# Kernel optimization log

Measured on AMD Instinct MI355X. Metric: run time of the kernel, lower is better.

The kernel has to match this reference:

```python
import jax, jax.numpy as jnp
import numpy as np

N_OBJ, N_EVT, N_EDGE, N_MAIN = 50000, 100000, 500000, 25000
OBJ_DIM, EVT_DIM = 256, 256


def setup_inputs() -> dict:
    key = jax.random.key(0)
    ks = jax.random.split(key, 12)
    s = 1.0 / np.sqrt(OBJ_DIM)
    return {
        "object_X": jax.random.normal(ks[0], (N_OBJ, OBJ_DIM), jnp.float32),
        "event_X": jax.random.normal(ks[1], (N_EVT, EVT_DIM), jnp.float32),
        "lc_obj_idx": jax.random.randint(ks[2], (N_EDGE,), 0, N_OBJ),
        "lc_evt_idx": jax.random.randint(ks[3], (N_EDGE,), 0, N_EVT),
        "main_idx": jax.random.randint(ks[4], (N_MAIN,), 0, N_OBJ),
        # lifecycle_proj: Linear(event_dim, obj_dim)
        "W_proj": jax.random.uniform(ks[5], (OBJ_DIM, EVT_DIM), jnp.float32, -s, s),
        "b_proj": jax.random.uniform(ks[6], (OBJ_DIM,), jnp.float32, -s, s),
        # GRUCell(obj_dim, obj_dim): weight_ih/hh are [3*H, H]
        "W_ih": jax.random.uniform(ks[7], (3 * OBJ_DIM, OBJ_DIM), jnp.float32, -s, s),
        "b_ih": jax.random.uniform(ks[8], (3 * OBJ_DIM,), jnp.float32, -s, s),
        "W_hh": jax.random.uniform(ks[9], (3 * OBJ_DIM, OBJ_DIM), jnp.float32, -s, s),
        "b_hh": jax.random.uniform(ks[10], (3 * OBJ_DIM,), jnp.float32, -s, s),
    }


def reference(object_X, event_X, lc_obj_idx, lc_evt_idx, main_idx,
              W_proj, b_proj, W_ih, b_ih, W_hh, b_hh):
    n_obj = object_X.shape[0]
    # gather event feats, linear + ReLU  -> [E, obj_dim]
    proj = jax.nn.relu(event_X[lc_evt_idx] @ W_proj.T + b_proj)
    # scatter_mean over target objects (empty slots -> 0, like torch_scatter)
    sums = jax.ops.segment_sum(proj, lc_obj_idx, num_segments=n_obj)
    cnt = jax.ops.segment_sum(jnp.ones((lc_obj_idx.shape[0],), proj.dtype),
                              lc_obj_idx, num_segments=n_obj)
    profile = sums / jnp.maximum(cnt, 1.0)[:, None]  # [N_obj, obj_dim]
    # GRUCell(profile, object_X)
    gi = profile @ W_ih.T + b_ih   # [N_obj, 3H]
    gh = object_X @ W_hh.T + b_hh  # [N_obj, 3H]
    i_r, i_z, i_n = jnp.split(gi, 3, axis=-1)
    h_r, h_z, h_n = jnp.split(gh, 3, axis=-1)
    r = jax.nn.sigmoid(i_r + h_r)
    z = jax.nn.sigmoid(i_z + h_z)
    n = jnp.tanh(i_n + r * h_n)
    updated = (1.0 - z) * n + z * object_X
    # masked blend: only main objects take updated values
    mask = jnp.zeros((n_obj, 1), object_X.dtype).at[main_idx].set(1.0)
    return mask * updated + (1.0 - mask) * object_X
```

## Files before the change

kernel.cpp:

```cpp
#include <hip/hip_runtime.h>

typedef unsigned short u16;
typedef __attribute__((ext_vector_type(8))) short bf16x8;
typedef __attribute__((ext_vector_type(4))) float f32x4;

struct __align__(8) u16x4_t { u16 x, y, z, w; };

__device__ __forceinline__ float b2f(u16 b) {
  union { unsigned u; float f; } v; v.u = ((unsigned)b) << 16; return v.f;
}
__device__ __forceinline__ u16 f2b(float f) {
  union { float f; unsigned u; } v; v.f = f;
  unsigned r = v.u + 0x7fffu + ((v.u >> 16) & 1u);
  return (u16)(r >> 16);
}
__device__ __forceinline__ unsigned pk2(float lo, float hi) {
  unsigned r;
  asm("v_cvt_pk_bf16_f32 %0, %1, %2" : "=v"(r) : "v"(lo), "v"(hi));
  return r;
}

__global__ void prep(const float* __restrict__ Wp, const float* __restrict__ Wi,
                     const float* __restrict__ Wh, u16* __restrict__ wb,
                     const int* __restrict__ main_idx, int* __restrict__ mask,
                     int* __restrict__ mlist, int* __restrict__ cpos,
                     int* __restrict__ mcount, int nMain) {
  int b = blockIdx.x;
  if (b < 448) {
    int t = b * 256 + threadIdx.x;
    const float* src; int o;
    if (t < 16384)      { src = Wp; o = t; }
    else if (t < 65536) { src = Wi; o = t - 16384; }
    else                { src = Wh; o = t - 65536; }
    float4 v = ((const float4*)src)[o];
    u16x4_t q;
    q.x = f2b(v.x); q.y = f2b(v.y); q.z = f2b(v.z); q.w = f2b(v.w);
    ((u16x4_t*)wb)[t] = q;
  } else {
    int t = (b - 448) * 256 + threadIdx.x;
    if (t < nMain) {
      int o = main_idx[t];
      if (atomicCAS(&mask[o], 0, 1) == 0) {
        int i = atomicAdd(mcount, 1);
        mlist[i] = o;
        cpos[o] = i;
      }
    }
  }
}

__global__ void count_edges(const int* __restrict__ obj_idx, const int* __restrict__ mask,
                            int* __restrict__ deg, int n) {
  int e = blockIdx.x * 256 + threadIdx.x;
  if (e >= n) return;
  int o = obj_idx[e];
  if (mask[o]) atomicAdd(&deg[o], 1);
}

__global__ __launch_bounds__(256)
void alloc_offs(const int* __restrict__ mlist, const int* __restrict__ mcount,
                const int* __restrict__ deg, int* __restrict__ offs,
                int* __restrict__ tcur, int* __restrict__ rrows, int Mpad) {
  int i = blockIdx.x * 256 + threadIdx.x;
  int lane = threadIdx.x & 63;
  int mc = *mcount;
  if (i < Mpad) rrows[i] = (i < mc) ? mlist[i] : 0;
  int o = (i < mc) ? mlist[i] : 0;
  int d = (i < mc) ? deg[o] : 0;
  int x = d;
#pragma unroll
  for (int s = 1; s < 64; s <<= 1) {
    int y = __shfl_up(x, s, 64);
    if (lane >= s) x += y;
  }
  int wt = __shfl(x, 63, 64);
  int base = 0;
  if (lane == 63 && wt > 0) base = atomicAdd(tcur, wt);
  base = __shfl(base, 63, 64);
  if (i < mc) offs[o] = base + (x - d);
}

__global__ void fill_edges(const int* __restrict__ obj_idx, const int* __restrict__ evt_idx,
                           const int* __restrict__ mask, const int* __restrict__ offs,
                           int* __restrict__ cursor, int* __restrict__ elist, int n) {
  int e = blockIdx.x * 256 + threadIdx.x;
  if (e >= n) return;
  int o = obj_idx[e];
  if (!mask[o]) return;
  int pos = atomicAdd(&cursor[o], 1);
  elist[offs[o] + pos] = evt_idx[e];
}

__global__ __launch_bounds__(256)
void accum_gather(const u16* __restrict__ P, const int* __restrict__ elist,
                  const int* __restrict__ offs, const int* __restrict__ deg,
                  const int* __restrict__ mlist, const int* __restrict__ mcount,
                  const float* __restrict__ objX, const int* __restrict__ rrows,
                  u16* __restrict__ prof, u16* __restrict__ objc, int Mpad) {
  const int wave = threadIdx.x >> 6;
  const int lane = threadIdx.x & 63;
  const int i = blockIdx.x * 4 + wave;
  if (i >= Mpad) return;

  int src = rrows[i];
  float4 xv = *(const float4*)(objX + (size_t)src * 256 + lane * 4);

  const int mc = *mcount;
  float a0 = 0.f, a1 = 0.f, a2 = 0.f, a3 = 0.f;
  int d = 0;
  if (i < mc) {
    const int o = mlist[i];
    const int off = offs[o];
    d = deg[o];
    int j = 0;
    for (; j + 1 < d; j += 2) {
      int e0 = elist[off + j], e1 = elist[off + j + 1];
      u16x4_t p0 = *(const u16x4_t*)(P + (size_t)e0 * 256 + lane * 4);
      u16x4_t p1 = *(const u16x4_t*)(P + (size_t)e1 * 256 + lane * 4);
      a0 += b2f(p0.x) + b2f(p1.x);
      a1 += b2f(p0.y) + b2f(p1.y);
      a2 += b2f(p0.z) + b2f(p1.z);
      a3 += b2f(p0.w) + b2f(p1.w);
    }
    if (j < d) {
      int e0 = elist[off + j];
      u16x4_t p0 = *(const u16x4_t*)(P + (size_t)e0 * 256 + lane * 4);
      a0 += b2f(p0.x); a1 += b2f(p0.y); a2 += b2f(p0.z); a3 += b2f(p0.w);
    }
  }
  float s = 1.f / fmaxf((float)d, 1.f);
  u16x4_t pv;
  pv.x = f2b(a0 * s); pv.y = f2b(a1 * s); pv.z = f2b(a2 * s); pv.w = f2b(a3 * s);
  *(u16x4_t*)(prof + (size_t)i * 256 + lane * 4) = pv;

  u16x4_t ov;
  ov.x = f2b(xv.x); ov.y = f2b(xv.y); ov.z = f2b(xv.z); ov.w = f2b(xv.w);
  *(u16x4_t*)(objc + (size_t)i * 256 + lane * 4) = ov;
}

template<int RELU>
__device__ __forceinline__
void gemm_core(const u16* __restrict__ A, const u16* __restrict__ B,
               const float* __restrict__ bias, u16* __restrict__ C,
               int M, int N, int n0, int m0, u16* lA, u16* lB) {
  const int tid  = threadIdx.x;
  const int lane = tid & 63;
  const int wave = tid >> 6;
  const int mR = (wave & 1) * 64;
  const int nC = (wave >> 1) * 64;

  int srow[4], skq[4];
#pragma unroll
  for (int s = 0; s < 4; ++s) {
    int g = s * 256 + tid;
    srow[s] = g >> 3;
    skq[s]  = ((g & 7) ^ ((g >> 3) & 7)) << 3;
  }

  f32x4 acc[4][4] = {};

  auto STAGE = [&](int buf, int kt) {
#pragma unroll
    for (int s = 0; s < 4; ++s) {
      int row = srow[s];
      int ar = m0 + row; ar = (ar < M) ? ar : (M - 1);
      const u16* gA = A + (size_t)ar * 256 + kt + skq[s];
      __builtin_amdgcn_global_load_lds(
          (const __attribute__((address_space(1))) void*)gA,
          (__attribute__((address_space(3))) void*)(lA + buf * 8192 + s * 2048 + wave * 512),
          16, 0, 0);
      const u16* gB = B + (size_t)(n0 + row) * 256 + kt + skq[s];
      __builtin_amdgcn_global_load_lds(
          (const __attribute__((address_space(1))) void*)gB,
          (__attribute__((address_space(3))) void*)(lB + buf * 8192 + s * 2048 + wave * 512),
          16, 0, 0);
    }
  };

  STAGE(0, 0);
  __syncthreads();

  for (int t = 0; t < 4; ++t) {
    const int cur = t & 1;
    if (t < 3) STAGE(cur ^ 1, (t + 1) * 64);
    const u16* bA = lA + cur * 8192;
    const u16* bB = lB + cur * 8192;
#pragma unroll
    for (int ks = 0; ks < 2; ++ks) {
      const int kbq = ks * 4 + (lane >> 4);
      bf16x8 af[4], bf[4];
#pragma unroll
      for (int i = 0; i < 4; ++i) {
        int ra = mR + i * 16 + (lane & 15);
        af[i] = *(const bf16x8*)(bA + ra * 64 + ((kbq ^ (ra & 7)) << 3));
        int rb = nC + i * 16 + (lane & 15);
        bf[i] = *(const bf16x8*)(bB + rb * 64 + ((kbq ^ (rb & 7)) << 3));
      }
#pragma unroll
      for (int i = 0; i < 4; ++i)
#pragma unroll
        for (int j = 0; j < 4; ++j)
          acc[i][j] = __builtin_amdgcn_mfma_f32_16x16x32_bf16(af[i], bf[j], acc[i][j], 0, 0, 0);
    }
    __syncthreads();
  }

  const int crow = (lane >> 4) * 4;
  const int ccol = lane & 15;
#pragma unroll
  for (int i = 0; i < 4; ++i) {
#pragma unroll
    for (int j = 0; j < 4; ++j) {
      int col = n0 + nC + j * 16 + ccol;
      float bv = bias[col];
#pragma unroll
      for (int q = 0; q < 4; ++q) {
        int row = m0 + mR + i * 16 + crow + q;
        if (row < M) {
          float v = acc[i][j][q] + bv;
          if (RELU) v = fmaxf(v, 0.f);
          C[(size_t)row * N + col] = f2b(v);
        }
      }
    }
  }
}

__device__ __forceinline__ int xcd_swz(int bid, int nwg) {
  int q = nwg >> 3, r = nwg & 7;
  int xcd = bid & 7, loc = bid >> 3;
  return (xcd < r ? xcd * (q + 1) : r * (q + 1) + (xcd - r) * q) + loc;
}

__global__ __launch_bounds__(256, 2)
void gemm_pf(const float* __restrict__ A, const u16* __restrict__ B,
             const float* __restrict__ bias, u16* __restrict__ C, int M) {
  __shared__ float lA[2][64 * 32];
  __shared__ u16   lB[2][128 * 64];
  const int tid  = threadIdx.x;
  const int lane = tid & 63;
  const int wave = tid >> 6;
  const int m0 = blockIdx.x * 64;
  const int nC = wave * 64;

  const float* asrc[2];
  const u16*   bsrc[4];
#pragma unroll
  for (int s = 0; s < 2; ++s) {
    int g = s * 256 + tid;
    int row = g >> 3, qp = g & 7;
    int q = qp ^ (row & 7);
    int ar = m0 + row; ar = (ar < M) ? ar : (M - 1);
    asrc[s] = A + (size_t)ar * 256 + q * 4;
  }
#pragma unroll
  for (int s = 0; s < 4; ++s) {
    int g = s * 256 + tid;
    int rp = g >> 3, qp = g & 7;
    int bq = qp ^ (rp & 7);
    int n  = rp * 2 + (bq >> 2);
    bsrc[s] = B + (size_t)n * 256 + (bq & 3) * 8;
  }

  auto STAGE = [&](int buf, int kt) {
#pragma unroll
    for (int s = 0; s < 2; ++s) {
      int g = s * 256 + tid;
      __builtin_amdgcn_global_load_lds(
          (const __attribute__((address_space(1))) void*)(asrc[s] + kt),
          (__attribute__((address_space(3))) void*)(&lA[buf][g * 4]),
          16, 0, 0);
    }
#pragma unroll
    for (int s = 0; s < 4; ++s) {
      int g = s * 256 + tid;
      __builtin_amdgcn_global_load_lds(
          (const __attribute__((address_space(1))) void*)(bsrc[s] + kt),
          (__attribute__((address_space(3))) void*)(&lB[buf][g * 8]),
          16, 0, 0);
    }
  };

  f32x4 acc[4][4] = {};
  STAGE(0, 0);
  __syncthreads();

  const int h = lane >> 4;
  for (int t = 0; t < 8; ++t) {
    const int cur = t & 1;
    if (t < 7) STAGE(cur ^ 1, (t + 1) * 32);
    const float* bA = lA[cur];
    const u16*   bB = lB[cur];
    bf16x8 af[4], bf[4];
#pragma unroll
    for (int i = 0; i < 4; ++i) {
      int ra = i * 16 + (lane & 15);
      int pg = (2 * h) ^ (ra & 7);
      float4 x = *(const float4*)(bA + ra * 32 + pg * 4);
      float4 y = *(const float4*)(bA + ra * 32 + (pg ^ 1) * 4);
      union { unsigned u[4]; bf16x8 v; } cv;
      cv.u[0] = pk2(x.x, x.y); cv.u[1] = pk2(x.z, x.w);
      cv.u[2] = pk2(y.x, y.y); cv.u[3] = pk2(y.z, y.w);
      af[i] = cv.v;
    }
#pragma unroll
    for (int j = 0; j < 4; ++j) {
      int rb = nC + j * 16 + (lane & 15);
      int qp = (((rb & 1) << 2) | h) ^ ((rb >> 1) & 7);
      bf[j] = *(const bf16x8*)(bB + (rb >> 1) * 64 + qp * 8);
    }
#pragma unroll
    for (int i = 0; i < 4; ++i)
#pragma unroll
      for (int j = 0; j < 4; ++j)
        acc[i][j] = __builtin_amdgcn_mfma_f32_16x16x32_bf16(af[i], bf[j], acc[i][j], 0, 0, 0);
    __syncthreads();
  }

  const int crow = (lane >> 4) * 4;
  const int ccol = lane & 15;
#pragma unroll
  for (int i = 0; i < 4; ++i) {
#pragma unroll
    for (int j = 0; j < 4; ++j) {
      int col = nC + j * 16 + ccol;
      float bv = bias[col];
#pragma unroll
      for (int q = 0; q < 4; ++q) {
        int row = m0 + i * 16 + crow + q;
        if (row < M)
          C[(size_t)row * 256 + col] = f2b(fmaxf(acc[i][j][q] + bv, 0.f));
      }
    }
  }
}

__global__ __launch_bounds__(256, 2)
void gemm2_dual(const u16* __restrict__ prof, const u16* __restrict__ objc,
                const u16* __restrict__ wib, const u16* __restrict__ whb,
                const float* __restrict__ bi, const float* __restrict__ bh,
                u16* __restrict__ gi, u16* __restrict__ gh, int Mpad, int nwg) {
  __shared__ u16 lA[2 * 8192];
  __shared__ u16 lB[2 * 8192];
  int wg = xcd_swz(blockIdx.x, nwg);
  int m0 = (wg / 12) * 128;
  int y = wg % 12;
  if (y < 6) gemm_core<0>(prof, wib, bi, gi, Mpad, 768, y * 128, m0, lA, lB);
  else       gemm_core<0>(objc, whb, bh, gh, Mpad, 768, (y - 6) * 128, m0, lA, lB);
}

__global__ __launch_bounds__(256)
void gate_out(const u16* __restrict__ gi, const u16* __restrict__ gh,
              const float* __restrict__ objX, const int* __restrict__ mask,
              const int* __restrict__ cpos, float* __restrict__ out, int nObj) {
  const int wave = threadIdx.x >> 6;
  const int lane = threadIdx.x & 63;
  const int row = blockIdx.x * 4 + wave;
  if (row >= nObj) return;
  float4 x4 = *(const float4*)(objX + (size_t)row * 256 + lane * 4);
  float4 r4 = x4;
  if (mask[row]) {
    size_t b = (size_t)cpos[row] * 768 + lane * 4;
    u16x4_t ir = *(const u16x4_t*)(gi + b);
    u16x4_t iz = *(const u16x4_t*)(gi + b + 256);
    u16x4_t in_ = *(const u16x4_t*)(gi + b + 512);
    u16x4_t hr = *(const u16x4_t*)(gh + b);
    u16x4_t hz = *(const u16x4_t*)(gh + b + 256);
    u16x4_t hn = *(const u16x4_t*)(gh + b + 512);
    float xs[4] = {x4.x, x4.y, x4.z, x4.w};
    u16 irs[4] = {ir.x, ir.y, ir.z, ir.w};
    u16 izs[4] = {iz.x, iz.y, iz.z, iz.w};
    u16 ins[4] = {in_.x, in_.y, in_.z, in_.w};
    u16 hrs[4] = {hr.x, hr.y, hr.z, hr.w};
    u16 hzs[4] = {hz.x, hz.y, hz.z, hz.w};
    u16 hns[4] = {hn.x, hn.y, hn.z, hn.w};
    float rs[4];
#pragma unroll
    for (int q = 0; q < 4; ++q) {
      float r = 1.f / (1.f + __expf(-(b2f(irs[q]) + b2f(hrs[q]))));
      float z = 1.f / (1.f + __expf(-(b2f(izs[q]) + b2f(hzs[q]))));
      float a = b2f(ins[q]) + r * b2f(hns[q]);
      float n = 1.f - 2.f / (__expf(2.f * a) + 1.f);
      rs[q] = (1.f - z) * n + z * xs[q];
    }
    r4.x = rs[0]; r4.y = rs[1]; r4.z = rs[2]; r4.w = rs[3];
  }
  *(float4*)(out + (size_t)row * 256 + lane * 4) = r4;
}


extern "C" void kernel_launch(void* const* d_in, const int* in_sizes, int n_in,
                              void* d_out, int out_size, void* d_ws, size_t ws_size,
                              hipStream_t stream) {
  const float* objX   = (const float*)d_in[0];
  const float* evtX   = (const float*)d_in[1];
  const int* obj_idx  = (const int*)d_in[2];
  const int* evt_idx  = (const int*)d_in[3];
  const int* main_idx = (const int*)d_in[4];
  const float* Wp = (const float*)d_in[5];
  const float* bp = (const float*)d_in[6];
  const float* Wi = (const float*)d_in[7];
  const float* bi = (const float*)d_in[8];
  const float* Wh = (const float*)d_in[9];
  const float* bh = (const float*)d_in[10];

  const int nObj  = in_sizes[0] / 256;
  const int nEvt  = in_sizes[1] / 256;
  const int nEdge = in_sizes[2];
  const int nMain = in_sizes[4];
  const int Mpad  = ((nMain + 127) / 128) * 128;

  char* ws = (char*)d_ws;
  u16*   P     = (u16*)(ws + 0);
  u16*   gi    = (u16*)(ws + 0);
  u16*   gh    = (u16*)(ws + 51200000);
  u16*   prof  = (u16*)(ws + 89735168);
  u16*   objc  = (u16*)(ws + 102580224);
  u16*   wb    = (u16*)(ws + 166625280);
  u16*   wpb   = wb;
  u16*   wib   = wb + 65536;
  u16*   whb   = wb + 262144;
  int*   deg   = (int*)(ws + 167542784);
  int*   cursor= (int*)(ws + 167742784);
  int*   mask  = (int*)(ws + 167942784);
  int*   mcount= (int*)(ws + 168142784);
  int*   tcur  = (int*)(ws + 168142848);
  int*   cpos  = (int*)(ws + 168142912);
  int*   offs  = (int*)(ws + 168342912);
  int*   mlist = (int*)(ws + 168542912);
  int*   rrows = (int*)(ws + 168643264);
  int*   elist = (int*)(ws + 168743616);
  float* out   = (float*)d_out;

  hipMemsetAsync(ws + 167542784, 0, 600128, stream);

  const int prepGrid = 448 + (nMain + 255) / 256;
  prep<<<prepGrid, 256, 0, stream>>>(Wp, Wi, Wh, wb,
                                     main_idx, mask, mlist, cpos, mcount, nMain);

  gemm_pf<<<(nEvt + 63) / 64, 256, 0, stream>>>(evtX, wpb, bp, P, nEvt);

  count_edges<<<(nEdge + 255) / 256, 256, 0, stream>>>(obj_idx, mask, deg, nEdge);
  alloc_offs<<<Mpad / 256, 256, 0, stream>>>(mlist, mcount, deg, offs, tcur, rrows, Mpad);
  fill_edges<<<(nEdge + 255) / 256, 256, 0, stream>>>(obj_idx, evt_idx, mask, offs, cursor, elist, nEdge);

  accum_gather<<<(Mpad + 3) / 4, 256, 0, stream>>>(P, elist, offs, deg, mlist, mcount,
                                                   objX, rrows, prof, objc, Mpad);

  const int nwg = (Mpad / 128) * 12;
  gemm2_dual<<<nwg, 256, 0, stream>>>(prof, objc, wib, whb, bi, bh, gi, gh, Mpad, nwg);

  gate_out<<<(nObj + 3) / 4, 256, 0, stream>>>(gi, gh, objX, mask, cpos, out, nObj);
}
```

Baseline: 381.1 us.

## Triple-buffer GEMM LDS staging with vmcnt waits and single barrier per k-step

Both GEMM kernels move from double-buffered LDS with two __syncthreads per iteration to a three-stage ring buffer. Loads are issued two steps ahead, and synchronization uses an explicit s_waitcnt vmcnt plus one s_barrier. The GEMM core also drops its k-tile from 64 to 32 and uses a 4-way XOR swizzle, which shrinks LDS per block. The goal is more overlap between global loads and MFMA work and fewer barrier stalls. The risk is that the hand-counted vmcnt values are fragile, and the smaller k-tile adds more iterations.

Result: no change. 379.5 us (-0.4%).

```diff
diff --git a/kernel.cpp b/kernel.cpp
--- a/kernel.cpp
+++ b/kernel.cpp
@@ -149,60 +149,61 @@
   const int mR = (wave & 1) * 64;
   const int nC = (wave >> 1) * 64;
 
-  int srow[4], skq[4];
-#pragma unroll
-  for (int s = 0; s < 4; ++s) {
+  const u16* asrc[2];
+  const u16* bsrc[2];
+#pragma unroll
+  for (int s = 0; s < 2; ++s) {
     int g = s * 256 + tid;
-    srow[s] = g >> 3;
-    skq[s]  = ((g & 7) ^ ((g >> 3) & 7)) << 3;
-  }
+    int row = g >> 2, qp = g & 3;
+    int q = qp ^ (row & 3);
+    int ar = m0 + row; ar = (ar < M) ? ar : (M - 1);
+    asrc[s] = A + (size_t)ar * 256 + q * 8;
+    bsrc[s] = B + (size_t)(n0 + row) * 256 + q * 8;
+  }
+
+  auto STAGE = [&](int buf, int kt) {
+#pragma unroll
+    for (int s = 0; s < 2; ++s) {
+      int g = s * 256 + tid;
+      __builtin_amdgcn_global_load_lds(
+          (const __attribute__((address_space(1))) void*)(asrc[s] + kt),
+          (__attribute__((address_space(3))) void*)(lA + buf * 4096 + g * 8),
+          16, 0, 0);
+      __builtin_amdgcn_global_load_lds(
+          (const __attribute__((address_space(1))) void*)(bsrc[s] + kt),
+          (__attribute__((address_space(3))) void*)(lB + buf * 4096 + g * 8),
+          16, 0, 0);
+    }
+  };
 
   f32x4 acc[4][4] = {};
-
-  auto STAGE = [&](int buf, int kt) {
-#pragma unroll
-    for (int s = 0; s < 4; ++s) {
-      int row = srow[s];
-      int ar = m0 + row; ar = (ar < M) ? ar : (M - 1);
-      const u16* gA = A + (size_t)ar * 256 + kt + skq[s];
-      __builtin_amdgcn_global_load_lds(
-          (const __attribute__((address_space(1))) void*)gA,
-          (__attribute__((address_space(3))) void*)(lA + buf * 8192 + s * 2048 + wave * 512),
-          16, 0, 0);
-      const u16* gB = B + (size_t)(n0 + row) * 256 + kt + skq[s];
-      __builtin_amdgcn_global_load_lds(
-          (const __attribute__((address_space(1))) void*)gB,
-          (__attribute__((address_space(3))) void*)(lB + buf * 8192 + s * 2048 + wave * 512),
-          16, 0, 0);
-    }
-  };
-
   STAGE(0, 0);
-  __syncthreads();
-
-  for (int t = 0; t < 4; ++t) {
-    const int cur = t & 1;
-    if (t < 3) STAGE(cur ^ 1, (t + 1) * 64);
-    const u16* bA = lA + cur * 8192;
-    const u16* bB = lB + cur * 8192;
-#pragma unroll
-    for (int ks = 0; ks < 2; ++ks) {
-      const int kbq = ks * 4 + (lane >> 4);
-      bf16x8 af[4], bf[4];
-#pragma unroll
-      for (int i = 0; i < 4; ++i) {
-        int ra = mR + i * 16 + (lane & 15);
-        af[i] = *(const bf16x8*)(bA + ra * 64 + ((kbq ^ (ra & 7)) << 3));
-        int rb = nC + i * 16 + (lane & 15);
-        bf[i] = *(const bf16x8*)(bB + rb * 64 + ((kbq ^ (rb & 7)) << 3));
-      }
-#pragma unroll
-      for (int i = 0; i < 4; ++i)
-#pragma unroll
-        for (int j = 0; j < 4; ++j)
-          acc[i][j] = __builtin_amdgcn_mfma_f32_16x16x32_bf16(af[i], bf[j], acc[i][j], 0, 0, 0);
-    }
-    __syncthreads();
+  STAGE(1, 32);
+
+  const int h = lane >> 4;
+#pragma unroll
+  for (int t = 0; t < 8; ++t) {
+    if (t < 7) asm volatile("s_waitcnt vmcnt(4)" ::: "memory");
+    else       asm volatile("s_waitcnt vmcnt(0)" ::: "memory");
+    __builtin_amdgcn_sched_barrier(0);
+    __builtin_amdgcn_s_barrier();
+    __builtin_amdgcn_sched_barrier(0);
+    const u16* bA = lA + (t % 3) * 4096;
+    const u16* bB = lB + (t % 3) * 4096;
+    bf16x8 af[4], bf[4];
+#pragma unroll
+    for (int i = 0; i < 4; ++i) {
+      int ra = mR + i * 16 + (lane & 15);
+      af[i] = *(const bf16x8*)(bA + ra * 32 + ((h ^ (ra & 3)) << 3));
+      int rb = nC + i * 16 + (lane & 15);
+      bf[i] = *(const bf16x8*)(bB + rb * 32 + ((h ^ (rb & 3)) << 3));
+    }
+#pragma unroll
+    for (int i = 0; i < 4; ++i)
+#pragma unroll
+      for (int j = 0; j < 4; ++j)
+        acc[i][j] = __builtin_amdgcn_mfma_f32_16x16x32_bf16(af[i], bf[j], acc[i][j], 0, 0, 0);
+    if (t < 6) STAGE((t + 2) % 3, (t + 2) * 32);
   }
 
   const int crow = (lane >> 4) * 4;
@@ -235,8 +236,8 @@
 __global__ __launch_bounds__(256, 2)
 void gemm_pf(const float* __restrict__ A, const u16* __restrict__ B,
              const float* __restrict__ bias, u16* __restrict__ C, int M) {
-  __shared__ float lA[2][64 * 32];
-  __shared__ u16   lB[2][128 * 64];
+  __shared__ float lA[3][64 * 32];
+  __shared__ u16   lB[3][256 * 32];
   const int tid  = threadIdx.x;
   const int lane = tid & 63;
   const int wave = tid >> 6;
@@ -256,10 +257,9 @@
 #pragma unroll
   for (int s = 0; s < 4; ++s) {
     int g = s * 256 + tid;
-    int rp = g >> 3, qp = g & 7;
-    int bq = qp ^ (rp & 7);
-    int n  = rp * 2 + (bq >> 2);
-    bsrc[s] = B + (size_t)n * 256 + (bq & 3) * 8;
+    int n = g >> 2, qp = g & 3;
+    int q = qp ^ (n & 3);
+    bsrc[s] = B + (size_t)n * 256 + q * 8;
   }
 
   auto STAGE = [&](int buf, int kt) {
@@ -283,14 +283,18 @@
 
   f32x4 acc[4][4] = {};
   STAGE(0, 0);
-  __syncthreads();
+  STAGE(1, 32);
 
   const int h = lane >> 4;
+#pragma unroll
   for (int t = 0; t < 8; ++t) {
-    const int cur = t & 1;
-    if (t < 7) STAGE(cur ^ 1, (t + 1) * 32);
-    const float* bA = lA[cur];
-    const u16*   bB = lB[cur];
+    if (t < 7) asm volatile("s_waitcnt vmcnt(6)" ::: "memory");
+    else       asm volatile("s_waitcnt vmcnt(0)" ::: "memory");
+    __builtin_amdgcn_sched_barrier(0);
+    __builtin_amdgcn_s_barrier();
+    __builtin_amdgcn_sched_barrier(0);
+    const float* bA = lA[t % 3];
+    const u16*   bB = lB[t % 3];
     bf16x8 af[4], bf[4];
 #pragma unroll
     for (int i = 0; i < 4; ++i) {
@@ -306,15 +310,14 @@
 #pragma unroll
     for (int j = 0; j < 4; ++j) {
       int rb = nC + j * 16 + (lane & 15);
-      int qp = (((rb & 1) << 2) | h) ^ ((rb >> 1) & 7);
-      bf[j] = *(const bf16x8*)(bB + (rb >> 1) * 64 + qp * 8);
+      bf[j] = *(const bf16x8*)(bB + rb * 32 + ((h ^ (rb & 3)) << 3));
     }
 #pragma unroll
     for (int i = 0; i < 4; ++i)
 #pragma unroll
       for (int j = 0; j < 4; ++j)
         acc[i][j] = __builtin_amdgcn_mfma_f32_16x16x32_bf16(af[i], bf[j], acc[i][j], 0, 0, 0);
-    __syncthreads();
+    if (t < 6) STAGE((t + 2) % 3, (t + 2) * 32);
   }
 
   const int crow = (lane >> 4) * 4;
@@ -340,8 +343,8 @@
                 const u16* __restrict__ wib, const u16* __restrict__ whb,
                 const float* __restrict__ bi, const float* __restrict__ bh,
                 u16* __restrict__ gi, u16* __restrict__ gh, int Mpad, int nwg) {
-  __shared__ u16 lA[2 * 8192];
-  __shared__ u16 lB[2 * 8192];
+  __shared__ u16 lA[3 * 4096];
+  __shared__ u16 lB[3 * 4096];
   int wg = xcd_swz(blockIdx.x, nwg);
   int m0 = (wg / 12) * 128;
   int y = wg % 12;
```
